# Kernel tuning notes

Hardware: AMD Instinct MI355X
Metric: run time of the kernel (lower is better)

The kernel has to match this reference:

```python
import jax, jax.numpy as jnp
import numpy as np

# ---- Cl(4,1) geometric-product Cayley table: gp(a,b)[k] = a[i] b[j] C[i,j,k] ----
def _build_cayley():
    metric = np.array([1.0, 1.0, 1.0, 1.0, -1.0], dtype=np.float32)  # signature (4,1)
    C = np.zeros((32, 32, 32), dtype=np.float32)
    for a in range(32):
        for b in range(32):
            # canonical reordering sign (count of swaps to merge blades)
            cnt = 0
            ash = a >> 1
            while ash:
                cnt += bin(ash & b).count('1')
                ash >>= 1
            s = -1.0 if (cnt & 1) else 1.0
            common = a & b
            for i in range(5):
                if (common >> i) & 1:
                    s *= metric[i]
            C[a, b, a ^ b] = s
    return C

CAYLEY = _build_cayley()
N_HEADS = 8

def gp_cl41(a, b, C):
    # a, b: (..., 32) multivectors
    return jnp.einsum('...i,...j,ijk->...k', a, b, C)

def normalize_cl41(x, eps=1e-6):
    n = jnp.sqrt(jnp.sum(x * x, axis=-1, keepdims=True) + eps)
    return x / n

def vlinear(x, w, b):
    # x: (..., Din, 32), w: (Dout, Din), b: (Dout, 32) -- blade-wise channel mixing
    return jnp.einsum('...ik,oi->...ok', x, w) + b

def layernorm2d(x, w, b, eps=1e-5):
    # normalized_shape = [D, 32]
    m = jnp.mean(x, axis=(-2, -1), keepdims=True)
    v = jnp.var(x, axis=(-2, -1), keepdims=True)
    return (x - m) / jnp.sqrt(v + eps) * w + b

def attention(x, wq, bq, wk, bk, wv, bv, wo, bo):
    B, S, D, K = x.shape
    hd = D // N_HEADS
    q = vlinear(x, wq, bq).reshape(B, S, N_HEADS, hd, K)
    k = vlinear(x, wk, bk).reshape(B, S, N_HEADS, hd, K)
    v = vlinear(x, wv, bv).reshape(B, S, N_HEADS, hd, K)
    scores = jnp.einsum('bqhdk,bshdk->bhqs', q, k) / jnp.sqrt(jnp.float32(hd * K))
    p = jax.nn.softmax(scores, axis=-1)
    o = jnp.einsum('bhqs,bshdk->bqhdk', p, v).reshape(B, S, D, K)
    return vlinear(o, wo, bo)


def setup_inputs() -> dict:
    key = jax.random.key(0)
    B, S, D, K = 4, 512, 256, 32
    L, E, NC = 2, 4, 1000
    ks = jax.random.split(key, 24)
    s = 1.0 / np.sqrt(D)
    inp = {
        'x': jax.random.normal(ks[0], (B, S, D, K), jnp.float32),
        'ln1_w': jnp.ones((L, D, K), jnp.float32),
        'ln1_b': jnp.zeros((L, D, K), jnp.float32),
        'wq': jax.random.normal(ks[1], (L, D, D), jnp.float32) * s,
        'bq': jnp.zeros((L, D, K), jnp.float32),
        'wk': jax.random.normal(ks[2], (L, D, D), jnp.float32) * s,
        'bk': jnp.zeros((L, D, K), jnp.float32),
        'wv': jax.random.normal(ks[3], (L, D, D), jnp.float32) * s,
        'bv': jnp.zeros((L, D, K), jnp.float32),
        'wo': jax.random.normal(ks[4], (L, D, D), jnp.float32) * s,
        'bo': jnp.zeros((L, D, K), jnp.float32),
        'ln2_w': jnp.ones((L, D, K), jnp.float32),
        'ln2_b': jnp.zeros((L, D, K), jnp.float32),
        'w1': jax.random.normal(ks[5], (L, E * D, D), jnp.float32) * s,
        'b1': jnp.zeros((L, E * D, K), jnp.float32),
        'w2': jax.random.normal(ks[6], (L, D, E * D), jnp.float32) * (1.0 / np.sqrt(E * D)),
        'b2': jnp.zeros((L, D, K), jnp.float32),
        'wr': jax.random.normal(ks[7], (D, D), jnp.float32) * s,
        'br': jnp.zeros((D, K), jnp.float32),
        'wc': jax.random.normal(ks[8], (NC, D * K), jnp.float32) * 0.02,
        'bc': jnp.zeros((NC,), jnp.float32),
    }
    return inp


def reference(x, ln1_w, ln1_b, wq, bq, wk, bk, wv, bv, wo, bo,
              ln2_w, ln2_b, w1, b1, w2, b2, wr, br, wc, bc):
    C = jnp.asarray(CAYLEY)
    L = ln1_w.shape[0]
    for l in range(L):
        h = layernorm2d(x, ln1_w[l], ln1_b[l])
        x = x + attention(h, wq[l], bq[l], wk[l], bk[l], wv[l], bv[l], wo[l], bo[l])
        x = normalize_cl41(x)
        h = layernorm2d(x, ln2_w[l], ln2_b[l])
        h = jnp.tanh(vlinear(h, w1[l], b1[l]))
        x = x + vlinear(h, w2[l], b2[l])
        x = normalize_cl41(x)
    # Recursive Rotor Accumulator pooling: psi_{t+1} = normalize(gp(r_t, psi_t))
    delta = vlinear(x, wr, br)                    # (B, S, D, 32)
    B, S, D, K = delta.shape
    psi0 = jnp.zeros((B, D, K), x.dtype).at[..., 0].set(1.0)
    def step(psi, r_t):
        return normalize_cl41(gp_cl41(r_t, psi, C)), None
    psi, _ = jax.lax.scan(step, psi0, jnp.moveaxis(delta, 1, 0))
    logits = psi.reshape(B, D * K) @ wc.T + bc
    return logits
```

## Files before the change

### kernel.cpp

```cpp
#include <hip/hip_runtime.h>
#include <hip/hip_bf16.h>
#include <cstdint>
#include <cstddef>

typedef __bf16 bf16_t;
typedef __attribute__((ext_vector_type(8))) __bf16 bf16x8;
typedef __attribute__((ext_vector_type(4))) __bf16 bf16x4;
typedef __attribute__((ext_vector_type(4))) float f32x4;

#define DEV __device__ __forceinline__

DEV void async16(const bf16_t* g, bf16_t* l) {
  __builtin_amdgcn_global_load_lds((const __attribute__((address_space(1))) void*)g,
                                   (__attribute__((address_space(3))) void*)l, 16, 0, 0);
}

DEV float fast_tanh(float x) {
  const float ex = __expf(2.f * x);
  return 1.f - 2.f / (ex + 1.f);
}

enum { EPI_RESID = 0, EPI_FFN1 = 1, EPI_QKV = 2, EPI_SCORE = 3, EPI_PV = 4, EPI_DELTAT = 5 };

template<int EPI, bool TRANSB>
__global__ __launch_bounds__(256, 2)
void gemm_k(const bf16_t* __restrict__ A, const bf16_t* __restrict__ A2,
            const bf16_t* __restrict__ B, const bf16_t* __restrict__ B2,
            const float* __restrict__ bias, void* __restrict__ outp, void* __restrict__ outp2,
            int Kd, int lda, int ldb, long aStride, long bStride)
{
  __shared__ bf16_t sA [2][4096];
  __shared__ bf16_t sB [2][4096];
  __shared__ bf16_t sA2[2][4096];
  __shared__ bf16_t sB2[2][4096];

  const int tid  = threadIdx.x;
  const int lane = tid & 63;
  const int wv   = tid >> 6;
  const int wr   = wv >> 1, wc = wv & 1;

  unsigned gx = gridDim.x, gy = gridDim.y;
  unsigned nb = gx * gy * gridDim.z;
  unsigned fid = blockIdx.x + gx * (blockIdx.y + gy * blockIdx.z);
  if ((nb & 7u) == 0u) fid = (fid & 7u) * (nb >> 3) + (fid >> 3);
  const unsigned bxu = fid % gx;
  const unsigned rem = fid / gx;
  const unsigned byu = rem % gy;
  const unsigned bzu = rem / gy;
  const int m0 = byu * 128;
  const int n0 = bxu * 128;
  const int bz = bzu;

  const bf16_t *Ab, *Bb, *A2b, *B2b;
  if constexpr (EPI == EPI_SCORE) {
    const int h = bz & 7;
    const long ho = (long)(bz >> 3) * 512;
    Ab  = A  + (long)h * aStride + ho;
    Bb  = B  + (long)h * bStride + ho;
    A2b = A2 + (long)h * aStride + ho;
    B2b = B2 + (long)h * bStride + ho;
  } else {
    Ab  = A  + (long)bz * aStride;
    Bb  = B  + (long)bz * bStride;
    A2b = A2 + (long)bz * aStride;
    B2b = B2 + (long)bz * bStride;
  }

  const int sRow = tid >> 2;
  const int sKo  = (tid & 3) * 8;
  const int tr = tid & 15;
  const int tc = tid >> 4;

  f32x4 acc[4][4];
#pragma unroll
  for (int i = 0; i < 4; i++)
#pragma unroll
    for (int j = 0; j < 4; j++) acc[i][j] = f32x4{0.f, 0.f, 0.f, 0.f};

  const int ns  = Kd >> 5;
  const int off = (int)(fid & (unsigned)(ns - 1));

  uint4 br0, br1, br2, br3;

  auto stageA = [&](int si, int b) {
    const int kt = ((si + off) & (ns - 1)) << 5;
    const bf16_t* ga  = Ab  + (long)(m0 + sRow) * lda + kt + sKo;
    const bf16_t* ga2 = A2b + (long)(m0 + sRow) * lda + kt + sKo;
    async16(ga,             &sA [b][tid * 8]);
    async16(ga + 64 * lda,  &sA [b][2048 + tid * 8]);
    async16(ga2,            &sA2[b][tid * 8]);
    async16(ga2 + 64 * lda, &sA2[b][2048 + tid * 8]);
  };
  auto stageB = [&](int si, int b) {
    const int kt = ((si + off) & (ns - 1)) << 5;
    const bf16_t* gb  = Bb  + (long)(n0 + sRow) * ldb + kt + sKo;
    const bf16_t* gb2 = B2b + (long)(n0 + sRow) * ldb + kt + sKo;
    async16(gb,             &sB [b][tid * 8]);
    async16(gb + 64 * ldb,  &sB [b][2048 + tid * 8]);
    async16(gb2,            &sB2[b][tid * 8]);
    async16(gb2 + 64 * ldb, &sB2[b][2048 + tid * 8]);
  };
  auto loadBR = [&](int si) {
    const int kt = ((si + off) & (ns - 1)) << 5;
    const bf16_t* gb  = Bb  + (long)(kt + tr) * ldb + n0 + tc * 8;
    const bf16_t* gb2 = B2b + (long)(kt + tr) * ldb + n0 + tc * 8;
    br0 = *(const uint4*)gb;
    br1 = *(const uint4*)(gb + 16 * ldb);
    br2 = *(const uint4*)gb2;
    br3 = *(const uint4*)(gb2 + 16 * ldb);
  };

  stageA(0, 0);
  if constexpr (!TRANSB) stageB(0, 0); else loadBR(0);

  for (int si = 0; si < ns; si++) {
    const int cb = si & 1;
    if (si + 1 < ns) stageA(si + 1, cb ^ 1);
    if constexpr (TRANSB) {
      const bf16_t* e0 = (const bf16_t*)&br0;
      const bf16_t* e1 = (const bf16_t*)&br1;
      const bf16_t* e2 = (const bf16_t*)&br2;
      const bf16_t* e3 = (const bf16_t*)&br3;
#pragma unroll
      for (int j = 0; j < 8; j++) {
        sB [cb][(tc * 8 + j) * 32 + tr]      = e0[j];
        sB [cb][(tc * 8 + j) * 32 + tr + 16] = e1[j];
        sB2[cb][(tc * 8 + j) * 32 + tr]      = e2[j];
        sB2[cb][(tc * 8 + j) * 32 + tr + 16] = e3[j];
      }
      if (si + 1 < ns) loadBR(si + 1);
      if (si + 1 >= ns) asm volatile("s_waitcnt vmcnt(0)" ::: "memory");
    } else {
      if (si + 1 < ns) {
        stageB(si + 1, cb ^ 1);
        asm volatile("s_waitcnt vmcnt(8)" ::: "memory");
      } else {
        asm volatile("s_waitcnt vmcnt(0)" ::: "memory");
      }
    }
    __syncthreads();

    bf16x8 af[4], bfr[4], af2[4], bf2[4];
#pragma unroll
    for (int i = 0; i < 4; i++) {
      const int ao = (wr * 64 + i * 16 + (lane & 15)) * 32 + (lane >> 4) * 8;
      const int bo = (wc * 64 + i * 16 + (lane & 15)) * 32 + (lane >> 4) * 8;
      af[i]  = *(const bf16x8*)&sA [cb][ao];
      af2[i] = *(const bf16x8*)&sA2[cb][ao];
      bfr[i] = *(const bf16x8*)&sB [cb][bo];
      bf2[i] = *(const bf16x8*)&sB2[cb][bo];
    }
#pragma unroll
    for (int i = 0; i < 4; i++)
#pragma unroll
      for (int j = 0; j < 4; j++) {
        acc[i][j] = __builtin_amdgcn_mfma_f32_16x16x32_bf16(af[i],  bfr[j], acc[i][j], 0, 0, 0);
        acc[i][j] = __builtin_amdgcn_mfma_f32_16x16x32_bf16(af[i],  bf2[j], acc[i][j], 0, 0, 0);
        acc[i][j] = __builtin_amdgcn_mfma_f32_16x16x32_bf16(af2[i], bfr[j], acc[i][j], 0, 0, 0);
      }
    __syncthreads();
  }

  const int cn = lane & 15;
  const int rg = (lane >> 4) * 4;
#pragma unroll
  for (int i = 0; i < 4; i++) {
    const int mb = m0 + wr * 64 + i * 16 + rg;
#pragma unroll
    for (int j = 0; j < 4; j++) {
      const int n = n0 + wc * 64 + j * 16 + cn;
#pragma unroll
      for (int r = 0; r < 4; r++) {
        const int m = mb + r;
        const float v = acc[i][j][r];
        if constexpr (EPI == EPI_RESID) {
          const float bb = bias ? bias[n * 32 + (m & 31)] : 0.f;
          ((float*)outp)[(long)m * 256 + n] += v + bb;
        } else if constexpr (EPI == EPI_QKV) {
          const int s = m >> 5, kb = m & 31;
          const int proj = n >> 8, col = n & 255;
          const int h = col >> 5, dd = col & 31;
          const long oidx = (long)proj * 4194304 + (long)(h * 512 + s) * 1024 + kb * 32 + dd;
          const float t = v + bias[n * 32 + kb];
          const bf16_t hh = (bf16_t)t;
          ((bf16_t*)outp)[oidx]  = hh;
          ((bf16_t*)outp2)[oidx] = (bf16_t)(t - (float)hh);
        } else if constexpr (EPI == EPI_SCORE) {
          const int h = bz & 7, half = bz >> 3;
          float* dst = half ? (float*)outp2 : (float*)outp;
          dst[(long)h * 262144 + (long)m * 512 + n] = v * (1.f / 32.f);
        } else if constexpr (EPI == EPI_PV) {
          const int kb = n >> 5, dd = n & 31;
          const long oidx = (long)(m * 32 + kb) * 256 + bz * 32 + dd;
          const bf16_t hh = (bf16_t)v;
          ((bf16_t*)outp)[oidx]  = hh;
          ((bf16_t*)outp2)[oidx] = (bf16_t)(v - (float)hh);
        } else {
          const int b = m >> 14, t = (m >> 5) & 511, kb = m & 31;
          ((float*)outp)[(((long)(b * 256 + n) * 512 + t) * 32) + kb] = v + bias[n * 32 + kb];
        }
      }
    }
  }
}

__global__ __launch_bounds__(256, 2)
void ffn_k(const bf16_t* __restrict__ Ah, const bf16_t* __restrict__ Al,
           const bf16_t* __restrict__ W1h_, const bf16_t* __restrict__ W1l_,
           const bf16_t* __restrict__ W2h_, const bf16_t* __restrict__ W2l_,
           const float* __restrict__ b1, const float* __restrict__ b2,
           float* __restrict__ XT)
{
  __shared__ bf16_t sAh[32 * 256], sAl[32 * 256];
  __shared__ bf16_t sW[4][4096];
  __shared__ bf16_t sHh[32 * 128], sHl[32 * 128];

  const int tid  = threadIdx.x;
  const int lane = tid & 63;
  const int wn   = tid >> 6;
  const int l15  = lane & 15;
  const int lg   = lane >> 4;
  const int m0   = blockIdx.x * 32;
  const int coff = blockIdx.x & 7;
  const int soff = (blockIdx.x >> 3) & 7;
  const int toff = (blockIdx.x >> 3) & 3;

#pragma unroll
  for (int r = 0; r < 4; r++) {
    const int idx = r * 256 + tid;
    const int row = idx >> 5, cp = idx & 31;
    const int c = cp ^ (row & 31);
    async16(Ah + (long)(m0 + row) * 256 + c * 8, sAh + idx * 8);
    async16(Al + (long)(m0 + row) * 256 + c * 8, sAl + idx * 8);
  }
  asm volatile("s_waitcnt vmcnt(0)" ::: "memory");
  __syncthreads();

  bf16_t* myW = &sW[wn][0];
  const int wrow1 = lane >> 2;
  const int wsrc  = ((lane & 3) ^ ((lane >> 2) & 3)) * 8;
  const int rpc   = (lg ^ (l15 & 3)) * 8;

  f32x4 acc2[2][4];
#pragma unroll
  for (int i = 0; i < 2; i++)
#pragma unroll
    for (int j = 0; j < 4; j++) acc2[i][j] = f32x4{0.f, 0.f, 0.f, 0.f};

#pragma unroll 1
  for (int cc = 0; cc < 8; cc++) {
    const int ch = (cc + coff) & 7;
    const bf16_t* W1h = W1h_ + (long)(ch * 128) * 256;
    const bf16_t* W1l = W1l_ + (long)(ch * 128) * 256;

    auto stageW1 = [&](int sp, int b) {
#pragma unroll
      for (int q = 0; q < 2; q++) {
        const long r = wn * 32 + q * 16 + wrow1;
        async16(W1h + r * 256 + sp * 32 + wsrc, myW + b * 2048 + q * 512 + lane * 8);
        async16(W1l + r * 256 + sp * 32 + wsrc, myW + b * 2048 + 1024 + q * 512 + lane * 8);
      }
    };
    auto stageW2 = [&](int tp) {
#pragma unroll
      for (int q = 0; q < 4; q++) {
        const long r = wn * 64 + q * 16 + wrow1;
        async16(W2h_ + r * 1024 + ch * 128 + tp * 32 + wsrc, myW + q * 512 + lane * 8);
        async16(W2l_ + r * 1024 + ch * 128 + tp * 32 + wsrc, myW + 2048 + q * 512 + lane * 8);
      }
    };

    stageW1(soff & 7, 0);
    f32x4 acc1[2][2];
#pragma unroll
    for (int i = 0; i < 2; i++)
#pragma unroll
      for (int j = 0; j < 2; j++) acc1[i][j] = f32x4{0.f, 0.f, 0.f, 0.f};

    for (int s = 0; s < 8; s++) {
      const int b = s & 1;
      const int sp = (s + soff) & 7;
      if (s < 7) {
        stageW1((s + 1 + soff) & 7, b ^ 1);
        asm volatile("s_waitcnt vmcnt(4)" ::: "memory");
      } else {
        asm volatile("s_waitcnt vmcnt(0)" ::: "memory");
      }
      bf16x8 a_h[2], a_l[2], w_h[2], w_l[2];
#pragma unroll
      for (int i = 0; i < 2; i++) {
        const int arow = i * 16 + l15;
        const int ac = (sp * 4 + lg) ^ (arow & 31);
        a_h[i] = *(const bf16x8*)&sAh[arow * 256 + ac * 8];
        a_l[i] = *(const bf16x8*)&sAl[arow * 256 + ac * 8];
      }
#pragma unroll
      for (int j = 0; j < 2; j++) {
        const int r = j * 16 + l15;
        w_h[j] = *(const bf16x8*)&myW[b * 2048 + r * 32 + rpc];
        w_l[j] = *(const bf16x8*)&myW[b * 2048 + 1024 + r * 32 + rpc];
      }
#pragma unroll
      for (int i = 0; i < 2; i++)
#pragma unroll
        for (int j = 0; j < 2; j++) {
          acc1[i][j] = __builtin_amdgcn_mfma_f32_16x16x32_bf16(w_h[j], a_h[i], acc1[i][j], 0, 0, 0);
          acc1[i][j] = __builtin_amdgcn_mfma_f32_16x16x32_bf16(w_h[j], a_l[i], acc1[i][j], 0, 0, 0);
          acc1[i][j] = __builtin_amdgcn_mfma_f32_16x16x32_bf16(w_l[j], a_h[i], acc1[i][j], 0, 0, 0);
        }
    }

    asm volatile("s_waitcnt lgkmcnt(0)" ::: "memory");
    stageW2(toff & 3);

#pragma unroll
    for (int i = 0; i < 2; i++) {
      const int m = i * 16 + l15;
      const int kb = (m0 + m) & 31;
#pragma unroll
      for (int j = 0; j < 2; j++) {
        const int u = wn * 4 + j * 2 + (lg >> 1);
        const int pu = u ^ (m & 7);
        const int base = m * 128 + pu * 8 + (lg & 1) * 4;
        const int ncol = wn * 32 + j * 16 + lg * 4;
        bf16x4 h4, l4;
#pragma unroll
        for (int rr = 0; rr < 4; rr++) {
          const float t = fast_tanh(acc1[i][j][rr] + b1[(ch * 128 + ncol + rr) * 32 + kb]);
          const bf16_t hh = (bf16_t)t;
          h4[rr] = hh;
          l4[rr] = (bf16_t)(t - (float)hh);
        }
        *(bf16x4*)&sHh[base] = h4;
        *(bf16x4*)&sHl[base] = l4;
      }
    }
    __syncthreads();

    for (int t = 0; t < 4; t++) {
      const int tp = (t + toff) & 3;
      asm volatile("s_waitcnt vmcnt(0)" ::: "memory");
      bf16x8 h_h[2], h_l[2], v_h[4], v_l[4];
#pragma unroll
      for (int i = 0; i < 2; i++) {
        const int hrow = i * 16 + l15;
        const int pu = (tp * 4 + lg) ^ (hrow & 7);
        h_h[i] = *(const bf16x8*)&sHh[hrow * 128 + pu * 8];
        h_l[i] = *(const bf16x8*)&sHl[hrow * 128 + pu * 8];
      }
#pragma unroll
      for (int j = 0; j < 4; j++) {
        const int r2 = j * 16 + l15;
        v_h[j] = *(const bf16x8*)&myW[r2 * 32 + rpc];
        v_l[j] = *(const bf16x8*)&myW[2048 + r2 * 32 + rpc];
      }
      if (t < 3) {
        asm volatile("s_waitcnt lgkmcnt(0)" ::: "memory");
        stageW2((t + 1 + toff) & 3);
      }
#pragma unroll
      for (int i = 0; i < 2; i++)
#pragma unroll
        for (int j = 0; j < 4; j++) {
          acc2[i][j] = __builtin_amdgcn_mfma_f32_16x16x32_bf16(h_h[i], v_h[j], acc2[i][j], 0, 0, 0);
          acc2[i][j] = __builtin_amdgcn_mfma_f32_16x16x32_bf16(h_h[i], v_l[j], acc2[i][j], 0, 0, 0);
          acc2[i][j] = __builtin_amdgcn_mfma_f32_16x16x32_bf16(h_l[i], v_h[j], acc2[i][j], 0, 0, 0);
        }
    }
    __syncthreads();
  }

#pragma unroll
  for (int i = 0; i < 2; i++)
#pragma unroll
    for (int j = 0; j < 4; j++) {
      const int n2 = wn * 64 + j * 16 + l15;
#pragma unroll
      for (int rr = 0; rr < 4; rr++) {
        const int m = m0 + i * 16 + lg * 4 + rr;
        XT[(long)m * 256 + n2] += acc2[i][j][rr] + b2[n2 * 32 + (m & 31)];
      }
    }
}

__global__ __launch_bounds__(256)
void transpose_k(const float* __restrict__ src, float* __restrict__ dst, int R, int C)
{
  __shared__ float t[32][33];
  const long boff = (long)blockIdx.z * R * C;
  const int r0 = blockIdx.y * 32, c0 = blockIdx.x * 32;
  const int tx = threadIdx.x & 31, ty = threadIdx.x >> 5;
#pragma unroll
  for (int i = 0; i < 32; i += 8)
    t[ty + i][tx] = src[boff + (long)(r0 + ty + i) * C + c0 + tx];
  __syncthreads();
#pragma unroll
  for (int i = 0; i < 32; i += 8)
    dst[boff + (long)(c0 + ty + i) * R + r0 + tx] = t[tx][ty + i];
}

DEV void hilo4(const f32x4 t, bf16x4& h, bf16x4& l) {
#pragma unroll
  for (int j = 0; j < 4; j++) {
    const bf16_t hh = (bf16_t)t[j];
    h[j] = hh;
    l[j] = (bf16_t)(t[j] - (float)hh);
  }
}

template<int MODE>
__global__ __launch_bounds__(256)
void nl_k(const float* __restrict__ X, float* __restrict__ Xo,
          const float* __restrict__ wT, const float* __restrict__ bT,
          bf16_t* __restrict__ oh, bf16_t* __restrict__ ol)
{
  const int row = blockIdx.x * 4 + (threadIdx.x >> 6);
  const int l   = threadIdx.x & 63;
  const float4* Xr = (const float4*)X + (long)row * 2048 + l;
  f32x4 v[32];
#pragma unroll
  for (int kb = 0; kb < 32; kb++) {
    const float4 t = Xr[kb * 64];
    v[kb] = f32x4{t.x, t.y, t.z, t.w};
  }
  if constexpr (MODE & 1) {
    f32x4 ss = f32x4{1e-6f, 1e-6f, 1e-6f, 1e-6f};
#pragma unroll
    for (int kb = 0; kb < 32; kb++) ss += v[kb] * v[kb];
    const f32x4 rs = f32x4{rsqrtf(ss[0]), rsqrtf(ss[1]), rsqrtf(ss[2]), rsqrtf(ss[3])};
#pragma unroll
    for (int kb = 0; kb < 32; kb++) v[kb] *= rs;
    if constexpr (MODE & 2) {
      float4* Xw = (float4*)Xo + (long)row * 2048 + l;
#pragma unroll
      for (int kb = 0; kb < 32; kb++)
        Xw[kb * 64] = float4{v[kb][0], v[kb][1], v[kb][2], v[kb][3]};
    }
  }
  if constexpr (MODE & 4) {
    float s = 0.f, s2 = 0.f;
#pragma unroll
    for (int kb = 0; kb < 32; kb++) {
      s  += (v[kb][0] + v[kb][1]) + (v[kb][2] + v[kb][3]);
      s2 += (v[kb][0] * v[kb][0] + v[kb][1] * v[kb][1]) +
            (v[kb][2] * v[kb][2] + v[kb][3] * v[kb][3]);
    }
#pragma unroll
    for (int o = 32; o > 0; o >>= 1) { s += __shfl_xor(s, o); s2 += __shfl_xor(s2, o); }
    const float mean = s * (1.f / 8192.f);
    const float var  = s2 * (1.f / 8192.f) - mean * mean;
    const float rstd = rsqrtf(var + 1e-5f);
    const float4* w4 = (const float4*)wT + l;
    const float4* b4 = (const float4*)bT + l;
#pragma unroll
    for (int kb = 0; kb < 32; kb++) {
      const float4 ww = w4[kb * 64];
      const float4 bb = b4[kb * 64];
      f32x4 t;
      t[0] = (v[kb][0] - mean) * rstd * ww.x + bb.x;
      t[1] = (v[kb][1] - mean) * rstd * ww.y + bb.y;
      t[2] = (v[kb][2] - mean) * rstd * ww.z + bb.z;
      t[3] = (v[kb][3] - mean) * rstd * ww.w + bb.w;
      bf16x4 h4, l4;
      hilo4(t, h4, l4);
      const long oi = (long)row * 8192 + kb * 256 + l * 4;
      *(bf16x4*)&oh[oi] = h4;
      *(bf16x4*)&ol[oi] = l4;
    }
  }
  if constexpr (MODE & 8) {
#pragma unroll
    for (int kb = 0; kb < 32; kb++) {
      bf16x4 h4, l4;
      hilo4(v[kb], h4, l4);
      const long oi = (long)row * 8192 + kb * 256 + l * 4;
      *(bf16x4*)&oh[oi] = h4;
      *(bf16x4*)&ol[oi] = l4;
    }
  }
}

__global__ __launch_bounds__(256)
void softmax_k(const float* __restrict__ SC, const float* __restrict__ SC2,
               bf16_t* __restrict__ Ph, bf16_t* __restrict__ Pl)
{
  const int row = blockIdx.x * 4 + (threadIdx.x >> 6);
  const int lane = threadIdx.x & 63;
  const float* s1 = SC  + (long)row * 512;
  const float* s2 = SC2 + (long)row * 512;
  float4 a = *(const float4*)&s1[lane * 4];
  float4 c = *(const float4*)&s1[256 + lane * 4];
  const float4 a2 = *(const float4*)&s2[lane * 4];
  const float4 c2 = *(const float4*)&s2[256 + lane * 4];
  a.x += a2.x; a.y += a2.y; a.z += a2.z; a.w += a2.w;
  c.x += c2.x; c.y += c2.y; c.z += c2.z; c.w += c2.w;
  float mx = fmaxf(fmaxf(fmaxf(a.x, a.y), fmaxf(a.z, a.w)),
                   fmaxf(fmaxf(c.x, c.y), fmaxf(c.z, c.w)));
#pragma unroll
  for (int o = 32; o > 0; o >>= 1) mx = fmaxf(mx, __shfl_xor(mx, o));
  float e[8] = {expf(a.x - mx), expf(a.y - mx), expf(a.z - mx), expf(a.w - mx),
                expf(c.x - mx), expf(c.y - mx), expf(c.z - mx), expf(c.w - mx)};
  float sum = ((e[0] + e[1]) + (e[2] + e[3])) + ((e[4] + e[5]) + (e[6] + e[7]));
#pragma unroll
  for (int o = 32; o > 0; o >>= 1) sum += __shfl_xor(sum, o);
  const float inv = 1.f / sum;
  bf16x4 h0, h1, l0, l1;
#pragma unroll
  for (int j = 0; j < 4; j++) {
    const float p0 = e[j] * inv, p1 = e[4 + j] * inv;
    h0[j] = (bf16_t)p0; l0[j] = (bf16_t)(p0 - (float)h0[j]);
    h1[j] = (bf16_t)p1; l1[j] = (bf16_t)(p1 - (float)h1[j]);
  }
  *(bf16x4*)&Ph[(long)row * 512 + lane * 4] = h0;
  *(bf16x4*)&Ph[(long)row * 512 + 256 + lane * 4] = h1;
  *(bf16x4*)&Pl[(long)row * 512 + lane * 4] = l0;
  *(bf16x4*)&Pl[(long)row * 512 + 256 + lane * 4] = l1;
}

constexpr float gpsign(int i, int j) {
  int cnt = 0;
  for (int s = 1; s < 5; s++) cnt += __builtin_popcount((i >> s) & j);
  float sgn = (cnt & 1) ? -1.f : 1.f;
  if ((i & j) & 16) sgn = -sgn;
  return sgn;
}

DEV void gp32(const float* __restrict__ a, const float* __restrict__ b, float* __restrict__ o) {
#pragma unroll
  for (int k = 0; k < 32; k++) {
    float s0 = 0.f, s1 = 0.f;
#pragma unroll
    for (int i = 0; i < 32; i += 2) {
      s0 = fmaf(gpsign(i, i ^ k) * a[i], b[i ^ k], s0);
      s1 = fmaf(gpsign(i + 1, (i + 1) ^ k) * a[i + 1], b[(i + 1) ^ k], s1);
    }
    o[k] = s0 + s1;
  }
}

__global__ __launch_bounds__(256)
void gptree_k(const float* __restrict__ dT, float* __restrict__ psiO)
{
  __shared__ float bufA[256 * 33];
  __shared__ float bufB[128 * 33];
  const int chain = blockIdx.x;
  const int t = threadIdx.x;
  const float* src = dT + (long)chain * (512 * 32);
  {
    float v[64];
    const float4* g = (const float4*)(src + t * 64);
#pragma unroll
    for (int i = 0; i < 16; i++) *(float4*)&v[i * 4] = g[i];
    float o[32];
    gp32(v + 32, v, o);
    float ss = 1e-6f;
#pragma unroll
    for (int k = 0; k < 32; k++) ss = fmaf(o[k], o[k], ss);
    const float rs = rsqrtf(ss);
#pragma unroll
    for (int k = 0; k < 32; k++) bufA[t * 33 + k] = o[k] * rs;
  }
  __syncthreads();
  int cur = 0;
#pragma unroll 1
  for (int P = 128; P >= 1; P >>= 1) {
    const float* in = cur ? bufB : bufA;
    float* ob = cur ? bufA : bufB;
    if (t < P) {
      float a[32], b[32], o[32];
#pragma unroll
      for (int c = 0; c < 32; c++) { b[c] = in[t * 66 + c]; a[c] = in[t * 66 + 33 + c]; }
      gp32(a, b, o);
      float ss = 1e-6f;
#pragma unroll
      for (int k = 0; k < 32; k++) ss = fmaf(o[k], o[k], ss);
      const float rs = rsqrtf(ss);
#pragma unroll
      for (int k = 0; k < 32; k++) ob[t * 33 + k] = o[k] * rs;
    }
    cur ^= 1;
    __syncthreads();
  }
  if (t < 32) psiO[(long)chain * 32 + t] = (cur ? bufB : bufA)[t];
}

__global__ __launch_bounds__(256)
void cls_k(const float* __restrict__ psi, const float* __restrict__ wcw,
           const float* __restrict__ bc, float* __restrict__ out)
{
  const int c = blockIdx.x;
  const int tid = threadIdx.x;
  float a0 = 0.f, a1 = 0.f, a2 = 0.f, a3 = 0.f;
  for (int i = tid * 4; i < 8192; i += 1024) {
    const float4 w  = *(const float4*)&wcw[(long)c * 8192 + i];
    const float4 p0 = *(const float4*)&psi[i];
    const float4 p1 = *(const float4*)&psi[8192 + i];
    const float4 p2 = *(const float4*)&psi[16384 + i];
    const float4 p3 = *(const float4*)&psi[24576 + i];
    a0 += w.x * p0.x + w.y * p0.y + w.z * p0.z + w.w * p0.w;
    a1 += w.x * p1.x + w.y * p1.y + w.z * p1.z + w.w * p1.w;
    a2 += w.x * p2.x + w.y * p2.y + w.z * p2.z + w.w * p2.w;
    a3 += w.x * p3.x + w.y * p3.y + w.z * p3.z + w.w * p3.w;
  }
#pragma unroll
  for (int o = 32; o > 0; o >>= 1) {
    a0 += __shfl_down(a0, o); a1 += __shfl_down(a1, o);
    a2 += __shfl_down(a2, o); a3 += __shfl_down(a3, o);
  }
  __shared__ float red[4][4];
  const int wv = tid >> 6;
  if ((tid & 63) == 0) { red[wv][0] = a0; red[wv][1] = a1; red[wv][2] = a2; red[wv][3] = a3; }
  __syncthreads();
  if (tid < 4) {
    const float r = red[0][tid] + red[1][tid] + red[2][tid] + red[3][tid] + bc[c];
    out[(long)tid * 1000 + c] = r;
  }
}

__global__ void split_k(const float* __restrict__ in, bf16_t* __restrict__ h,
                        bf16_t* __restrict__ l, int n)
{
  const int i = blockIdx.x * 256 + threadIdx.x;
  if (i < n) {
    const float v = in[i];
    const bf16_t hh = (bf16_t)v;
    h[i] = hh;
    l[i] = (bf16_t)(v - (float)hh);
  }
}

__global__ void cpy_k(const float* __restrict__ in, float* __restrict__ o, int n)
{
  const int i = blockIdx.x * 256 + threadIdx.x;
  if (i < n) o[i] = in[i];
}

extern "C" void kernel_launch(void* const* d_in, const int* in_sizes, int n_in,
                              void* d_out, int out_size, void* d_ws, size_t ws_size,
                              hipStream_t stream)
{
  const float* x    = (const float*)d_in[0];
  const float* ln1w = (const float*)d_in[1];
  const float* ln1b = (const float*)d_in[2];
  const float* wq   = (const float*)d_in[3];
  const float* bq   = (const float*)d_in[4];
  const float* wk   = (const float*)d_in[5];
  const float* bk   = (const float*)d_in[6];
  const float* wvv  = (const float*)d_in[7];
  const float* bv   = (const float*)d_in[8];
  const float* wo   = (const float*)d_in[9];
  const float* bo   = (const float*)d_in[10];
  const float* ln2w = (const float*)d_in[11];
  const float* ln2b = (const float*)d_in[12];
  const float* w1   = (const float*)d_in[13];
  const float* b1   = (const float*)d_in[14];
  const float* w2   = (const float*)d_in[15];
  const float* b2   = (const float*)d_in[16];
  const float* wr   = (const float*)d_in[17];
  const float* br   = (const float*)d_in[18];
  const float* wcw  = (const float*)d_in[19];
  const float* bc   = (const float*)d_in[20];
  float* out = (float*)d_out;

  char* ws = (char*)d_ws;
  const size_t MB = 1ull << 20;
  const size_t KB = 1024;
  float*  XT   = (float*)(ws + 0);
  bf16_t* HBh  = (bf16_t*)(ws + 64 * MB);
  bf16_t* HBl  = (bf16_t*)(ws + 96 * MB);
  bf16_t* QKVh = (bf16_t*)(ws + 128 * MB);
  bf16_t* QKVl = (bf16_t*)(ws + 152 * MB);
  float*  SCb  = (float*)(ws + 176 * MB);
  float*  SC2b = (float*)(ws + 184 * MB);
  bf16_t* Ph   = QKVh;
  bf16_t* Pl   = QKVl;
  bf16_t* OBh  = QKVh + 4194304;
  bf16_t* OBl  = QKVl + 4194304;
  bf16_t* Vh   = QKVh + 8388608;
  bf16_t* Vl   = QKVl + 8388608;
  bf16_t* XHI = (bf16_t*)(ws + 64 * MB), *XLO = (bf16_t*)(ws + 96 * MB);
  float*  DELTAT = (float*)(ws + 128 * MB);
  float*  PSI  = (float*)(ws + 192 * MB);
  char*   W    = ws + 193 * MB;
  bf16_t* WQKVh = (bf16_t*)(W);
  bf16_t* WQKVl = (bf16_t*)(W + 1 * MB);
  bf16_t* W1h = (bf16_t*)(W + 2 * MB);   bf16_t* W1l = (bf16_t*)(W + 3 * MB);
  bf16_t* W2h = (bf16_t*)(W + 4 * MB);   bf16_t* W2l = (bf16_t*)(W + 5 * MB);
  bf16_t* WOh = (bf16_t*)(W + 6 * MB);   bf16_t* WOl = (bf16_t*)(W + 6 * MB + 256 * KB);
  bf16_t* WRh = (bf16_t*)(W + 6 * MB + 512 * KB);
  bf16_t* WRl = (bf16_t*)(W + 6 * MB + 640 * KB);
  float*  BQKV = (float*)(W + 6 * MB + 768 * KB);
  float*  LNT  = (float*)(W + 6 * MB + 960 * KB);
  float* LN1WT = LNT, *LN1BT = LNT + 16384, *LN2WT = LNT + 32768, *LN2BT = LNT + 49152;

  for (int l = 0; l < 2; l++) {
    split_k<<<256, 256, 0, stream>>>(wq + l * 65536, WQKVh + l * 196608, WQKVl + l * 196608, 65536);
    split_k<<<256, 256, 0, stream>>>(wk + l * 65536, WQKVh + l * 196608 + 65536, WQKVl + l * 196608 + 65536, 65536);
    split_k<<<256, 256, 0, stream>>>(wvv + l * 65536, WQKVh + l * 196608 + 131072, WQKVl + l * 196608 + 131072, 65536);
    cpy_k<<<32, 256, 0, stream>>>(bq + l * 8192, BQKV + l * 24576, 8192);
    cpy_k<<<32, 256, 0, stream>>>(bk + l * 8192, BQKV + l * 24576 + 8192, 8192);
    cpy_k<<<32, 256, 0, stream>>>(bv + l * 8192, BQKV + l * 24576 + 16384, 8192);
  }
  split_k<<<512, 256, 0, stream>>>(wo, WOh, WOl, 131072);
  split_k<<<2048, 256, 0, stream>>>(w1, W1h, W1l, 524288);
  split_k<<<2048, 256, 0, stream>>>(w2, W2h, W2l, 524288);
  split_k<<<256, 256, 0, stream>>>(wr, WRh, WRl, 65536);
  transpose_k<<<dim3(1, 8, 2), 256, 0, stream>>>(ln1w, LN1WT, 256, 32);
  transpose_k<<<dim3(1, 8, 2), 256, 0, stream>>>(ln1b, LN1BT, 256, 32);
  transpose_k<<<dim3(1, 8, 2), 256, 0, stream>>>(ln2w, LN2WT, 256, 32);
  transpose_k<<<dim3(1, 8, 2), 256, 0, stream>>>(ln2b, LN2BT, 256, 32);

  transpose_k<<<dim3(1, 8, 2048), 256, 0, stream>>>(x, XT, 256, 32);

  for (int l = 0; l < 2; l++) {
    if (l == 0)
      nl_k<4><<<512, 256, 0, stream>>>(XT, nullptr, LN1WT, LN1BT, HBh, HBl);
    for (int b = 0; b < 4; b++) {
      const long ao = (long)b * 16384 * 256;
      gemm_k<EPI_QKV, false><<<dim3(6, 128, 1), 256, 0, stream>>>(
          HBh + ao, HBl + ao, WQKVh + l * 196608, WQKVl + l * 196608,
          BQKV + l * 24576, QKVh, QKVl, 256, 256, 256, 0, 0);
      gemm_k<EPI_SCORE, false><<<dim3(4, 4, 16), 256, 0, stream>>>(
          QKVh, QKVl, QKVh + 4194304, QKVl + 4194304,
          nullptr, SCb, SC2b, 512, 1024, 1024, 512 * 1024, 512 * 1024);
      softmax_k<<<1024, 256, 0, stream>>>(SCb, SC2b, Ph, Pl);
      gemm_k<EPI_PV, true><<<dim3(8, 4, 8), 256, 0, stream>>>(
          Ph, Pl, Vh, Vl, nullptr, OBh, OBl, 512, 512, 1024, 512 * 512, 512 * 1024);
      gemm_k<EPI_RESID, false><<<dim3(2, 128, 1), 256, 0, stream>>>(
          OBh, OBl, WOh + l * 65536, WOl + l * 65536,
          bo + l * 8192, (float*)XT + ao, nullptr, 256, 256, 256, 0, 0);
    }
    nl_k<1 | 2 | 4><<<512, 256, 0, stream>>>(XT, XT, LN2WT + l * 8192, LN2BT + l * 8192, HBh, HBl);
    ffn_k<<<2048, 256, 0, stream>>>(HBh, HBl,
                                    W1h + l * 262144, W1l + l * 262144,
                                    W2h + l * 262144, W2l + l * 262144,
                                    b1 + l * 32768, b2 + l * 8192, XT);
    if (l == 0) {
      nl_k<1 | 2 | 4><<<512, 256, 0, stream>>>(XT, XT, LN1WT + 8192, LN1BT + 8192, HBh, HBl);
    } else {
      nl_k<1 | 8><<<512, 256, 0, stream>>>(XT, nullptr, nullptr, nullptr, XHI, XLO);
    }
  }

  gemm_k<EPI_DELTAT, false><<<dim3(2, 512, 1), 256, 0, stream>>>(
      XHI, XLO, WRh, WRl, br, DELTAT, nullptr, 256, 256, 256, 0, 0);
  gptree_k<<<1024, 256, 0, stream>>>(DELTAT, PSI);
  cls_k<<<1000, 256, 0, stream>>>(PSI, wcw, bc, out);
}
```

Measured before the change: 1.912 ms.

## Add A-resident small-tile GEMM kernel for K=256 projections

Adds a new GEMM kernel that stages a whole 32x256 A tile in LDS once and streams the weight operand in double-buffered 32-wide K slices per wave, with XOR swizzling and a staggered start slice per block. The QKV, output-projection and final rotor-delta GEMMs move to this kernel using 32x128 tiles and four times as many blocks, and the generic GEMM loses those epilogues. The aim is more parallelism and less A reloading for these K=256 GEMMs, at the cost of smaller tiles and more weight traffic per output.

```diff
diff --git a/kernel.cpp b/kernel.cpp
--- a/kernel.cpp
+++ b/kernel.cpp
@@ -173,19 +173,7 @@
       for (int r = 0; r < 4; r++) {
         const int m = mb + r;
         const float v = acc[i][j][r];
-        if constexpr (EPI == EPI_RESID) {
-          const float bb = bias ? bias[n * 32 + (m & 31)] : 0.f;
-          ((float*)outp)[(long)m * 256 + n] += v + bb;
-        } else if constexpr (EPI == EPI_QKV) {
-          const int s = m >> 5, kb = m & 31;
-          const int proj = n >> 8, col = n & 255;
-          const int h = col >> 5, dd = col & 31;
-          const long oidx = (long)proj * 4194304 + (long)(h * 512 + s) * 1024 + kb * 32 + dd;
-          const float t = v + bias[n * 32 + kb];
-          const bf16_t hh = (bf16_t)t;
-          ((bf16_t*)outp)[oidx]  = hh;
-          ((bf16_t*)outp2)[oidx] = (bf16_t)(t - (float)hh);
-        } else if constexpr (EPI == EPI_SCORE) {
+        if constexpr (EPI == EPI_SCORE) {
           const int h = bz & 7, half = bz >> 3;
           float* dst = half ? (float*)outp2 : (float*)outp;
           dst[(long)h * 262144 + (long)m * 512 + n] = v * (1.f / 32.f);
@@ -195,13 +183,121 @@
           const bf16_t hh = (bf16_t)v;
           ((bf16_t*)outp)[oidx]  = hh;
           ((bf16_t*)outp2)[oidx] = (bf16_t)(v - (float)hh);
+        }
+      }
+    }
+  }
+}
+
+template<int EPI>
+__global__ __launch_bounds__(256, 2)
+void awgemm_k(const bf16_t* __restrict__ Ah, const bf16_t* __restrict__ Al,
+              const bf16_t* __restrict__ Wh, const bf16_t* __restrict__ Wl,
+              const float* __restrict__ bias, void* __restrict__ outp, void* __restrict__ outp2)
+{
+  __shared__ bf16_t sAh[32 * 256], sAl[32 * 256];
+  __shared__ bf16_t sW[4][4096];
+
+  const int tid  = threadIdx.x;
+  const int lane = tid & 63;
+  const int wn   = tid >> 6;
+  const int l15  = lane & 15;
+  const int lg   = lane >> 4;
+  const int n0   = blockIdx.x * 128;
+  const int m0   = blockIdx.y * 32;
+  const int soff = (blockIdx.y ^ blockIdx.x) & 7;
+
+#pragma unroll
+  for (int r = 0; r < 4; r++) {
+    const int idx = r * 256 + tid;
+    const int row = idx >> 5, cp = idx & 31;
+    const int c = cp ^ (row & 31);
+    async16(Ah + (long)(m0 + row) * 256 + c * 8, sAh + idx * 8);
+    async16(Al + (long)(m0 + row) * 256 + c * 8, sAl + idx * 8);
+  }
+  asm volatile("s_waitcnt vmcnt(0)" ::: "memory");
+  __syncthreads();
+
+  bf16_t* myW = &sW[wn][0];
+  const int wrow1 = lane >> 2;
+  const int wsrc  = ((lane & 3) ^ ((lane >> 2) & 3)) * 8;
+  const int rpc   = (lg ^ (l15 & 3)) * 8;
+
+  auto stageW = [&](int sp, int b) {
+#pragma unroll
+    for (int q = 0; q < 2; q++) {
+      const long r = n0 + wn * 32 + q * 16 + wrow1;
+      async16(Wh + r * 256 + sp * 32 + wsrc, myW + b * 2048 + q * 512 + lane * 8);
+      async16(Wl + r * 256 + sp * 32 + wsrc, myW + b * 2048 + 1024 + q * 512 + lane * 8);
+    }
+  };
+
+  f32x4 acc[2][2];
+#pragma unroll
+  for (int i = 0; i < 2; i++)
+#pragma unroll
+    for (int j = 0; j < 2; j++) acc[i][j] = f32x4{0.f, 0.f, 0.f, 0.f};
+
+  stageW(soff & 7, 0);
+  for (int s = 0; s < 8; s++) {
+    const int b = s & 1;
+    const int sp = (s + soff) & 7;
+    if (s < 7) {
+      stageW((s + 1 + soff) & 7, b ^ 1);
+      asm volatile("s_waitcnt vmcnt(4)" ::: "memory");
+    } else {
+      asm volatile("s_waitcnt vmcnt(0)" ::: "memory");
+    }
+    bf16x8 a_h[2], a_l[2], w_h[2], w_l[2];
+#pragma unroll
+    for (int i = 0; i < 2; i++) {
+      const int arow = i * 16 + l15;
+      const int ac = (sp * 4 + lg) ^ (arow & 31);
+      a_h[i] = *(const bf16x8*)&sAh[arow * 256 + ac * 8];
+      a_l[i] = *(const bf16x8*)&sAl[arow * 256 + ac * 8];
+    }
+#pragma unroll
+    for (int j = 0; j < 2; j++) {
+      const int r = j * 16 + l15;
+      w_h[j] = *(const bf16x8*)&myW[b * 2048 + r * 32 + rpc];
+      w_l[j] = *(const bf16x8*)&myW[b * 2048 + 1024 + r * 32 + rpc];
+    }
+#pragma unroll
+    for (int i = 0; i < 2; i++)
+#pragma unroll
+      for (int j = 0; j < 2; j++) {
+        acc[i][j] = __builtin_amdgcn_mfma_f32_16x16x32_bf16(a_h[i], w_h[j], acc[i][j], 0, 0, 0);
+        acc[i][j] = __builtin_amdgcn_mfma_f32_16x16x32_bf16(a_h[i], w_l[j], acc[i][j], 0, 0, 0);
+        acc[i][j] = __builtin_amdgcn_mfma_f32_16x16x32_bf16(a_l[i], w_h[j], acc[i][j], 0, 0, 0);
+      }
+  }
+
+#pragma unroll
+  for (int i = 0; i < 2; i++)
+#pragma unroll
+    for (int j = 0; j < 2; j++) {
+      const int n = n0 + wn * 32 + j * 16 + l15;
+#pragma unroll
+      for (int rr = 0; rr < 4; rr++) {
+        const int m = m0 + i * 16 + lg * 4 + rr;
+        const float v = acc[i][j][rr];
+        if constexpr (EPI == EPI_QKV) {
+          const int s = m >> 5, kb = m & 31;
+          const int proj = n >> 8, col = n & 255;
+          const int h = col >> 5, dd = col & 31;
+          const long oidx = (long)proj * 4194304 + (long)(h * 512 + s) * 1024 + kb * 32 + dd;
+          const float t = v + bias[n * 32 + kb];
+          const bf16_t hh = (bf16_t)t;
+          ((bf16_t*)outp)[oidx]  = hh;
+          ((bf16_t*)outp2)[oidx] = (bf16_t)(t - (float)hh);
+        } else if constexpr (EPI == EPI_RESID) {
+          ((float*)outp)[(long)m * 256 + n] += v + bias[n * 32 + (m & 31)];
         } else {
           const int b = m >> 14, t = (m >> 5) & 511, kb = m & 31;
           ((float*)outp)[(((long)(b * 256 + n) * 512 + t) * 32) + kb] = v + bias[n * 32 + kb];
         }
       }
     }
-  }
 }
 
 __global__ __launch_bounds__(256, 2)
@@ -717,18 +813,18 @@
       nl_k<4><<<512, 256, 0, stream>>>(XT, nullptr, LN1WT, LN1BT, HBh, HBl);
     for (int b = 0; b < 4; b++) {
       const long ao = (long)b * 16384 * 256;
-      gemm_k<EPI_QKV, false><<<dim3(6, 128, 1), 256, 0, stream>>>(
+      awgemm_k<EPI_QKV><<<dim3(6, 512), 256, 0, stream>>>(
           HBh + ao, HBl + ao, WQKVh + l * 196608, WQKVl + l * 196608,
-          BQKV + l * 24576, QKVh, QKVl, 256, 256, 256, 0, 0);
+          BQKV + l * 24576, QKVh, QKVl);
       gemm_k<EPI_SCORE, false><<<dim3(4, 4, 16), 256, 0, stream>>>(
           QKVh, QKVl, QKVh + 4194304, QKVl + 4194304,
           nullptr, SCb, SC2b, 512, 1024, 1024, 512 * 1024, 512 * 1024);
       softmax_k<<<1024, 256, 0, stream>>>(SCb, SC2b, Ph, Pl);
       gemm_k<EPI_PV, true><<<dim3(8, 4, 8), 256, 0, stream>>>(
           Ph, Pl, Vh, Vl, nullptr, OBh, OBl, 512, 512, 1024, 512 * 512, 512 * 1024);
-      gemm_k<EPI_RESID, false><<<dim3(2, 128, 1), 256, 0, stream>>>(
+      awgemm_k<EPI_RESID><<<dim3(2, 512), 256, 0, stream>>>(
           OBh, OBl, WOh + l * 65536, WOl + l * 65536,
-          bo + l * 8192, (float*)XT + ao, nullptr, 256, 256, 256, 0, 0);
+          bo + l * 8192, (float*)XT + ao, nullptr);
     }
     nl_k<1 | 2 | 4><<<512, 256, 0, stream>>>(XT, XT, LN2WT + l * 8192, LN2BT + l * 8192, HBh, HBl);
     ffn_k<<<2048, 256, 0, stream>>>(HBh, HBl,
@@ -742,8 +838,8 @@
     }
   }
 
-  gemm_k<EPI_DELTAT, false><<<dim3(2, 512, 1), 256, 0, stream>>>(
-      XHI, XLO, WRh, WRl, br, DELTAT, nullptr, 256, 256, 256, 0, 0);
+  awgemm_k<EPI_DELTAT><<<dim3(2, 2048), 256, 0, stream>>>(
+      XHI, XLO, WRh, WRl, br, DELTAT, nullptr);
   gptree_k<<<1024, 256, 0, stream>>>(DELTAT, PSI);
   cls_k<<<1000, 256, 0, stream>>>(PSI, wcw, bc, out);
 }
```

Result: no change. 1.919 ms (+0.4%).
